# Performance work log

Measured on AMD Instinct MI355X. Metric: run time of the kernel, lower is better.

The kernel has to match this reference:

```python
import jax, jax.numpy as jnp
import numpy as np

EPS = 1e-5

def _ln(x, g, b):
    mu = jnp.mean(x, -1, keepdims=True)
    var = jnp.mean(jnp.square(x - mu), -1, keepdims=True)
    return (x - mu) * jax.lax.rsqrt(var + EPS) * g + b

def _switch_moe(h, gw, gb, W1, b1, W2, b2):
    # h: [B,T,D]; top-1 switch routing over E experts
    probs = jax.nn.softmax(h @ gw + gb, axis=-1)        # [B,T,E]
    idx = jnp.argmax(probs, axis=-1)                    # [B,T]
    p = jnp.max(probs, axis=-1)[..., None]              # [B,T,1] top-1 gate prob
    out = jnp.zeros_like(h)
    E = W1.shape[0]
    for e in range(E):  # small fixed expert count
        y = jax.nn.gelu(h @ W1[e] + b1[e]) @ W2[e] + b2[e]
        out = out + jnp.where((idx == e)[..., None], p * y, 0.0)
    return out

def setup_inputs() -> dict:
    key = jax.random.key(0)
    B, T, D, F, E, TE, NB = 64, 196, 512, 2048, 8, 512, 2
    ks = jax.random.split(key, 16)
    s = 0.02
    return {
        "x": jax.random.normal(ks[0], (B, T, D), jnp.float32),
        "emb": jax.random.normal(ks[1], (B, TE), jnp.float32),
        "ln_g": jnp.ones((NB, D), jnp.float32),
        "ln_b": jnp.zeros((NB, D), jnp.float32),
        "gate_w": jax.random.normal(ks[2], (NB, D, E), jnp.float32) * s,
        "gate_b": jnp.zeros((NB, E), jnp.float32),
        "w1": jax.random.normal(ks[3], (NB, E, D, F), jnp.float32) * s,
        "b1": jnp.zeros((NB, E, F), jnp.float32),
        "w2": jax.random.normal(ks[4], (NB, E, F, D), jnp.float32) * s,
        "b2": jnp.zeros((NB, E, D), jnp.float32),
        "emb_w": jax.random.normal(ks[5], (TE, 2 * D), jnp.float32) * s,
        "emb_b": jnp.zeros((2 * D,), jnp.float32),
        "sn_g": jnp.ones((D,), jnp.float32),
        "sn_b": jnp.zeros((D,), jnp.float32),
        "out_w": jax.random.normal(ks[6], (D, D), jnp.float32) * s,
        "out_b": jnp.zeros((D,), jnp.float32),
    }

def reference(x, emb, ln_g, ln_b, gate_w, gate_b, w1, b1, w2, b2,
              emb_w, emb_b, sn_g, sn_b, out_w, out_b):
    NB = ln_g.shape[0]
    out = jnp.zeros_like(x)
    for br in range(NB):  # fixed small branch count; dropout = identity (eval)
        h = _ln(x, ln_g[br], ln_b[br])
        out = out + _switch_moe(h, gate_w[br], gate_b[br], w1[br], b1[br], w2[br], b2[br])
    out = out / NB
    # StylizationBlock (FiLM): norm, scale/shift from time emb, SiLU+Linear, residual
    eo = jax.nn.silu(emb) @ emb_w + emb_b            # [B,2D]
    scale, shift = jnp.split(eo[:, None, :], 2, axis=-1)  # [B,1,D] each
    h = _ln(out, sn_g, sn_b) * (1.0 + scale) + shift
    h = jax.nn.silu(h) @ out_w + out_b
    return x + h
```

## Files before the change

kernel.cpp:

```cpp
#include <hip/hip_runtime.h>
#include <hip/hip_bf16.h>

typedef unsigned short u16;
typedef unsigned int u32;

typedef short bf16v8 __attribute__((ext_vector_type(8)));
typedef float f32v4 __attribute__((ext_vector_type(4)));

constexpr int BB   = 64;
constexpr int TT   = 196;
constexpr int NTOK = BB * TT;
constexpr int DD   = 512;
constexpr int FF   = 2048;
constexpr int EE   = 8;
constexpr int NBR  = 2;
constexpr int GE   = NBR * EE;
constexpr int MT128 = 212;
constexpr int NB_FRONT = 840 + NTOK / 4;

__device__ __forceinline__ u16 f2bf(float f) {
    union { float f; u32 u; } v; v.f = f;
    u32 r = v.u + 0x7fffu + ((v.u >> 16) & 1u);
    return (u16)(r >> 16);
}

__device__ __forceinline__ float bf2f(u32 u) {
    union { u32 u; float f; } v; v.u = u << 16; return v.f;
}

__device__ __forceinline__ float wave_sum(float v) {
    #pragma unroll
    for (int m = 32; m > 0; m >>= 1) v += __shfl_xor(v, m, 64);
    return v;
}

__device__ __forceinline__ float gelu_tanh(float v) {
    float y = 1.595769122f * v + 0.071354816f * (v * v * v);
    return v / (1.0f + __expf(-y));
}

__device__ __forceinline__ float silu(float v) {
    return v / (1.0f + __expf(-v));
}

__device__ __forceinline__ void gload16(const u16* g, u16* l) {
    typedef const __attribute__((address_space(1))) unsigned gv_t;
    typedef __attribute__((address_space(3))) unsigned lv_t;
    __builtin_amdgcn_global_load_lds((gv_t*)g, (lv_t*)l, 16, 0, 0);
}

__device__ __forceinline__ void bar() {
    asm volatile("" ::: "memory");
    __builtin_amdgcn_s_barrier();
    asm volatile("" ::: "memory");
}

#define ASM_VMCNT4 asm volatile("s_waitcnt vmcnt(4)" ::: "memory")
#define ASM_VMCNT0 asm volatile("s_waitcnt vmcnt(0)" ::: "memory")
#define ASM_LGKM0  asm volatile("s_waitcnt lgkmcnt(0)" ::: "memory")

__global__ __launch_bounds__(256) void front_kernel(
    const float* __restrict__ w1, u16* __restrict__ w1t,
    const float* __restrict__ w2, u16* __restrict__ w2t,
    const float* __restrict__ ow, u16* __restrict__ owt,
    const float* __restrict__ emb, const float* __restrict__ emb_w,
    const float* __restrict__ emb_b, float* __restrict__ eo,
    int* __restrict__ cnt,
    const float* __restrict__ x, const float* __restrict__ ln_g,
    const float* __restrict__ ln_b, const float* __restrict__ gate_w,
    const float* __restrict__ gate_b,
    u16* __restrict__ hA, u16* __restrict__ hB,
    int* __restrict__ idxb, float* __restrict__ pbuf)
{
    __shared__ __align__(16) float smem[2 * 64 * 69];
    int id = blockIdx.x;
    int t = threadIdx.x;

    if (id >= 840) {
        int wave = t >> 6, lane = t & 63;
        int tok = (id - 840) * 4 + wave;
        const float* xr = x + (size_t)tok * DD + lane * 8;
        float4 v0 = *(const float4*)xr;
        float4 v1 = *(const float4*)(xr + 4);
        float xs[8] = {v0.x, v0.y, v0.z, v0.w, v1.x, v1.y, v1.z, v1.w};
        float s = 0.f, ss = 0.f;
        #pragma unroll
        for (int i = 0; i < 8; ++i) { s += xs[i]; ss += xs[i] * xs[i]; }
        s = wave_sum(s); ss = wave_sum(ss);
        float mu = s * (1.0f / DD);
        float var = ss * (1.0f / DD) - mu * mu;
        float rstd = rsqrtf(var + 1e-5f);

        #pragma unroll
        for (int br = 0; br < NBR; ++br) {
            u16* hb = br ? hB : hA;
            float part[8] = {0, 0, 0, 0, 0, 0, 0, 0};
            u16 hu[8];
            #pragma unroll
            for (int i = 0; i < 8; ++i) {
                int d = lane * 8 + i;
                float g = ln_g[br * DD + d], b = ln_b[br * DD + d];
                float h = (xs[i] - mu) * rstd * g + b;
                hu[i] = f2bf(h);
                const float* gw = gate_w + ((size_t)br * DD + d) * EE;
                float4 g0 = *(const float4*)gw;
                float4 g1 = *(const float4*)(gw + 4);
                part[0] += h * g0.x; part[1] += h * g0.y; part[2] += h * g0.z; part[3] += h * g0.w;
                part[4] += h * g1.x; part[5] += h * g1.y; part[6] += h * g1.z; part[7] += h * g1.w;
            }
            uint4 pk;
            pk.x = (u32)hu[0] | ((u32)hu[1] << 16);
            pk.y = (u32)hu[2] | ((u32)hu[3] << 16);
            pk.z = (u32)hu[4] | ((u32)hu[5] << 16);
            pk.w = (u32)hu[6] | ((u32)hu[7] << 16);
            *(uint4*)(hb + (size_t)tok * DD + lane * 8) = pk;

            float logit[8];
            #pragma unroll
            for (int e = 0; e < 8; ++e)
                logit[e] = wave_sum(part[e]) + gate_b[br * EE + e];
            float m = logit[0]; int bi = 0;
            #pragma unroll
            for (int e = 1; e < 8; ++e)
                if (logit[e] > m) { m = logit[e]; bi = e; }
            float sum = 0.f;
            #pragma unroll
            for (int e = 0; e < 8; ++e) sum += __expf(logit[e] - m);
            if (lane == 0) {
                idxb[br * NTOK + tok] = bi;
                pbuf[br * NTOK + tok] = 1.0f / sum;
            }
        }
        return;
    }

    if (id >= 776) {
        float* se = smem;
        int id2 = id - 776;
        int cg = id2 & 3, bg = id2 >> 2;
        int b0 = bg * 4;
        int c0 = cg * 256 + t;
        for (int i = t; i < 4 * DD; i += 256) {
            int b = i >> 9, d = i & (DD - 1);
            se[b * DD + d] = silu(emb[(size_t)(b0 + b) * DD + d]);
        }
        __syncthreads();
        float acc[4] = {0, 0, 0, 0};
        for (int k = 0; k < DD; ++k) {
            float wv = emb_w[(size_t)k * 1024 + c0];
            #pragma unroll
            for (int b = 0; b < 4; ++b) acc[b] += se[b * DD + k] * wv;
        }
        float bb = emb_b[c0];
        #pragma unroll
        for (int b = 0; b < 4; ++b)
            eo[(size_t)(b0 + b) * 1024 + c0] = acc[b] + bb;
        return;
    }

    if (id == 0 && t < 16) cnt[t] = 0;

    const float* src; u16* dst; int C, Rfull, rowbase, c0, NIT;
    if (id < 512) {
        int e = id >> 5, cg = id & 31;
        src = w1 + (size_t)e * DD * FF; dst = w1t + (size_t)e * FF * DD;
        C = FF; Rfull = DD; rowbase = 0; c0 = cg * 64; NIT = 8;
    } else if (id < 768) {
        int sid = id - 512; int e = sid >> 4, rem = sid & 15;
        src = w2 + (size_t)e * FF * DD; dst = w2t + (size_t)e * FF * DD;
        C = DD; Rfull = FF; rowbase = (rem >> 3) * 1024; c0 = (rem & 7) * 64; NIT = 16;
    } else {
        int cg = id - 768;
        src = ow; dst = owt;
        C = DD; Rfull = DD; rowbase = 0; c0 = cg * 64; NIT = 8;
    }

    float (*tile)[64][69] = (float (*)[64][69])smem;
    int tx = t & 15, ty = t >> 4;
    int wc = t & 7, wr0 = t >> 3;

    {
        float4 v[4];
        #pragma unroll
        for (int j = 0; j < 4; ++j)
            v[j] = *(const float4*)&src[(size_t)(rowbase + ty + 16 * j) * C + c0 + tx * 4];
        #pragma unroll
        for (int j = 0; j < 4; ++j) {
            int row = ty + 16 * j;
            tile[0][row][tx * 4 + 0] = v[j].x;
            tile[0][row][tx * 4 + 1] = v[j].y;
            tile[0][row][tx * 4 + 2] = v[j].z;
            tile[0][row][tx * 4 + 3] = v[j].w;
        }
        __syncthreads();
    }

    for (int it = 0; it < NIT; ++it) {
        int cur = it & 1;
        bool pre = (it + 1 < NIT);
        float4 nv[4];
        if (pre) {
            #pragma unroll
            for (int j = 0; j < 4; ++j)
                nv[j] = *(const float4*)&src[(size_t)(rowbase + (it + 1) * 64 + ty + 16 * j) * C + c0 + tx * 4];
        }
        #pragma unroll
        for (int p = 0; p < 2; ++p) {
            int cc = wr0 + p * 32;
            u16 pk[8];
            #pragma unroll
            for (int i = 0; i < 8; ++i)
                pk[i] = f2bf(tile[cur][wc * 8 + i][cc]);
            uint4 vv;
            vv.x = (u32)pk[0] | ((u32)pk[1] << 16);
            vv.y = (u32)pk[2] | ((u32)pk[3] << 16);
            vv.z = (u32)pk[4] | ((u32)pk[5] << 16);
            vv.w = (u32)pk[6] | ((u32)pk[7] << 16);
            *(uint4*)&dst[(size_t)(c0 + cc) * Rfull + rowbase + it * 64 + wc * 8] = vv;
        }
        if (pre) {
            #pragma unroll
            for (int j = 0; j < 4; ++j) {
                int row = ty + 16 * j;
                tile[cur ^ 1][row][tx * 4 + 0] = nv[j].x;
                tile[cur ^ 1][row][tx * 4 + 1] = nv[j].y;
                tile[cur ^ 1][row][tx * 4 + 2] = nv[j].z;
                tile[cur ^ 1][row][tx * 4 + 3] = nv[j].w;
            }
        }
        __syncthreads();
    }
}

__global__ __launch_bounds__(256) void route_kernel(
    const int* __restrict__ idxb, int* __restrict__ cnt, int* __restrict__ list)
{
    __shared__ int lcnt[GE];
    __shared__ int gbase[GE];
    int tid = threadIdx.x;
    int t = blockIdx.x * 256 + tid;
    if (tid < GE) lcnt[tid] = 0;
    __syncthreads();
    int e0 = idxb[t];
    int e1 = EE + idxb[NTOK + t];
    int r0 = atomicAdd(&lcnt[e0], 1);
    int r1 = atomicAdd(&lcnt[e1], 1);
    __syncthreads();
    if (tid < GE) {
        int c = lcnt[tid];
        gbase[tid] = c ? atomicAdd(&cnt[tid], c) : 0;
    }
    __syncthreads();
    list[(size_t)e0 * NTOK + gbase[e0] + r0] = t;
    list[(size_t)e1 * NTOK + gbase[e1] + r1] = t;
}

__global__ void tilestart_kernel(const int* __restrict__ cnt, int* __restrict__ meta)
{
    int lane = threadIdx.x;
    if (lane < 16) {
        int pbv = 0;
        for (int k = 0; k < lane; ++k) pbv += cnt[k];
        meta[lane] = pbv;
    }
    if (lane == 16) {
        int n = 0;
        for (int k = 0; k < 16; ++k) n += (cnt[k] + 127) >> 7;
        meta[33] = n;
    }
    for (int j = lane; j < MT128; j += 64) {
        int ge = -1, start = 0, tt = 0;
        #pragma unroll
        for (int k = 0; k < 16; ++k) {
            int mt = (cnt[k] + 127) >> 7;
            if (ge < 0) {
                if (j < start + mt) { ge = k; tt = j - start; }
                else start += mt;
            }
        }
        if (ge >= 0) meta[64 + j] = (ge << 20) | tt;
    }
}

template<int MODE>
__global__ __launch_bounds__(256, 4) void gemm_tile(
    const u16* __restrict__ A0, const u16* __restrict__ A1,
    const u16* __restrict__ Bt,
    const int* __restrict__ meta, const int* __restrict__ cnt,
    const int* __restrict__ list, const float* __restrict__ pbuf,
    const float* __restrict__ bias,
    u16* __restrict__ uout, u16* __restrict__ moeout)
{
    constexpr int K = (MODE == 1) ? FF : DD;
    constexpr int N = (MODE == 0) ? FF : DD;
    constexpr int NSTEP = K / 32;

    __shared__ __align__(16) u16 As[2][128 * 32];
    __shared__ __align__(16) u16 Bs[2][128 * 32];
    __shared__ int rowtok[128];
    __shared__ float rowp[128];

    int ntile = blockIdx.x;
    int j = blockIdx.y;
    if (j >= meta[33]) return;
    int ev = meta[64 + j];
    int ge = ev >> 20;
    int rb = (ev & 0xfffff) << 7;
    int cnt_e = cnt[ge];
    int pb = meta[ge];

    int tid = threadIdx.x, wave = tid >> 6, lane = tid & 63;
    int wm = wave >> 1, wn = wave & 1;
    int fr = lane & 15, fq = lane >> 4;
    int r0 = wave * 16 + (lane >> 2);
    int sc = (lane & 3) ^ ((lane >> 3) & 3);

    const u16* Abase;
    if constexpr (MODE == 0) Abase = (ge >= 8) ? A1 : A0;
    else                     Abase = A0;
    const u16* Bte = Bt + (size_t)ge * FF * DD;

    const u16 *aSrc0, *aSrc1, *bSrc0, *bSrc1;
    if constexpr (MODE == 0) {
        int lb = ge * NTOK;
        int g0 = rb + r0, g1 = g0 + 64;
        int t0 = (g0 < cnt_e) ? list[lb + g0] : list[lb];
        int t1 = (g1 < cnt_e) ? list[lb + g1] : list[lb];
        aSrc0 = Abase + (size_t)t0 * K + sc * 8;
        aSrc1 = Abase + (size_t)t1 * K + sc * 8;
    } else {
        size_t base = (size_t)(pb + rb);
        aSrc0 = Abase + (base + r0) * (size_t)K + sc * 8;
        aSrc1 = Abase + (base + r0 + 64) * (size_t)K + sc * 8;
    }
    {
        int nrow = ntile * 128 + r0;
        bSrc0 = Bte + (size_t)nrow * K + sc * 8;
        bSrc1 = Bte + (size_t)(nrow + 64) * K + sc * 8;
    }

    if constexpr (MODE == 1) {
        if (tid < 128) {
            int g = rb + tid;
            int tk = (g < cnt_e) ? list[ge * NTOK + g] : -1;
            rowtok[tid] = tk;
            rowp[tid] = (tk >= 0) ? pbuf[(ge >> 3) * NTOK + tk] : 0.f;
        }
        ASM_LGKM0;
    }

    f32v4 acc[4][4];
    #pragma unroll
    for (int mi = 0; mi < 4; ++mi)
        #pragma unroll
        for (int ni = 0; ni < 4; ++ni)
            acc[mi][ni] = (f32v4){0.f, 0.f, 0.f, 0.f};

    int ch = fq ^ ((fr >> 1) & 3);

    gload16(aSrc0, &As[0][wave * 512]);
    gload16(aSrc1, &As[0][2048 + wave * 512]);
    gload16(bSrc0, &Bs[0][wave * 512]);
    gload16(bSrc1, &Bs[0][2048 + wave * 512]);
    aSrc0 += 32; aSrc1 += 32; bSrc0 += 32; bSrc1 += 32;

    #pragma unroll 2
    for (int t = 0; t < NSTEP; ++t) {
        const int cur = t & 1;
        if (t + 1 < NSTEP) {
            gload16(aSrc0, &As[cur ^ 1][wave * 512]);
            gload16(aSrc1, &As[cur ^ 1][2048 + wave * 512]);
            gload16(bSrc0, &Bs[cur ^ 1][wave * 512]);
            gload16(bSrc1, &Bs[cur ^ 1][2048 + wave * 512]);
            aSrc0 += 32; aSrc1 += 32; bSrc0 += 32; bSrc1 += 32;
            ASM_VMCNT4;
        } else {
            ASM_VMCNT0;
        }
        bar();

        bf16v8 af[4], bfr[4];
        #pragma unroll
        for (int mi = 0; mi < 4; ++mi)
            af[mi] = *(const bf16v8*)&As[cur][(wm * 64 + mi * 16 + fr) * 32 + ch * 8];
        #pragma unroll
        for (int ni = 0; ni < 4; ++ni)
            bfr[ni] = *(const bf16v8*)&Bs[cur][(wn * 64 + ni * 16 + fr) * 32 + ch * 8];
        #pragma unroll
        for (int mi = 0; mi < 4; ++mi)
            #pragma unroll
            for (int ni = 0; ni < 4; ++ni)
                acc[mi][ni] = __builtin_amdgcn_mfma_f32_16x16x32_bf16(
                    af[mi], bfr[ni], acc[mi][ni], 0, 0, 0);
        bar();
    }

    #pragma unroll
    for (int mi = 0; mi < 4; ++mi) {
        #pragma unroll
        for (int ni = 0; ni < 4; ++ni) {
            int col = ntile * 128 + wn * 64 + ni * 16 + fr;
            float bn = bias[(size_t)ge * N + col];
            #pragma unroll
            for (int r = 0; r < 4; ++r) {
                int rr = wm * 64 + mi * 16 + fq * 4 + r;
                float v = acc[mi][ni][r] + bn;
                if constexpr (MODE == 0) {
                    if (rb + rr < cnt_e)
                        uout[(size_t)(pb + rb + rr) * FF + col] = f2bf(gelu_tanh(v));
                } else {
                    int tok = rowtok[rr];
                    if (tok >= 0)
                        moeout[((size_t)(ge >> 3) * NTOK + tok) * DD + col] =
                            f2bf(v * rowp[rr]);
                }
            }
        }
    }
}

__global__ __launch_bounds__(256, 4) void gemm_out(
    const u16* __restrict__ A0, const u16* __restrict__ Bt,
    const float* __restrict__ bias,
    const float* __restrict__ xres, float* __restrict__ dout)
{
    constexpr int K = DD;
    constexpr int NSTEP = K / 32;

    __shared__ __align__(16) u16 As[2][128 * 32];
    __shared__ __align__(16) u16 Bs[2][128 * 32];

    int ntile = blockIdx.x;
    int rb = blockIdx.y * 128;

    int tid = threadIdx.x, wave = tid >> 6, lane = tid & 63;
    int wm = wave >> 1, wn = wave & 1;
    int fr = lane & 15, fq = lane >> 4;
    int r0 = wave * 16 + (lane >> 2);
    int sc = (lane & 3) ^ ((lane >> 3) & 3);

    const u16 *aSrc0, *aSrc1, *bSrc0, *bSrc1;
    aSrc0 = A0 + (size_t)(rb + r0) * K + sc * 8;
    aSrc1 = A0 + (size_t)(rb + r0 + 64) * K + sc * 8;
    {
        int nrow = ntile * 128 + r0;
        bSrc0 = Bt + (size_t)nrow * K + sc * 8;
        bSrc1 = Bt + (size_t)(nrow + 64) * K + sc * 8;
    }

    f32v4 acc[4][4];
    #pragma unroll
    for (int mi = 0; mi < 4; ++mi)
        #pragma unroll
        for (int ni = 0; ni < 4; ++ni)
            acc[mi][ni] = (f32v4){0.f, 0.f, 0.f, 0.f};

    int ch = fq ^ ((fr >> 1) & 3);

    gload16(aSrc0, &As[0][wave * 512]);
    gload16(aSrc1, &As[0][2048 + wave * 512]);
    gload16(bSrc0, &Bs[0][wave * 512]);
    gload16(bSrc1, &Bs[0][2048 + wave * 512]);
    aSrc0 += 32; aSrc1 += 32; bSrc0 += 32; bSrc1 += 32;

    #pragma unroll 2
    for (int t = 0; t < NSTEP; ++t) {
        const int cur = t & 1;
        if (t + 1 < NSTEP) {
            gload16(aSrc0, &As[cur ^ 1][wave * 512]);
            gload16(aSrc1, &As[cur ^ 1][2048 + wave * 512]);
            gload16(bSrc0, &Bs[cur ^ 1][wave * 512]);
            gload16(bSrc1, &Bs[cur ^ 1][2048 + wave * 512]);
            aSrc0 += 32; aSrc1 += 32; bSrc0 += 32; bSrc1 += 32;
            ASM_VMCNT4;
        } else {
            ASM_VMCNT0;
        }
        bar();

        bf16v8 af[4], bfr[4];
        #pragma unroll
        for (int mi = 0; mi < 4; ++mi)
            af[mi] = *(const bf16v8*)&As[cur][(wm * 64 + mi * 16 + fr) * 32 + ch * 8];
        #pragma unroll
        for (int ni = 0; ni < 4; ++ni)
            bfr[ni] = *(const bf16v8*)&Bs[cur][(wn * 64 + ni * 16 + fr) * 32 + ch * 8];
        #pragma unroll
        for (int mi = 0; mi < 4; ++mi)
            #pragma unroll
            for (int ni = 0; ni < 4; ++ni)
                acc[mi][ni] = __builtin_amdgcn_mfma_f32_16x16x32_bf16(
                    af[mi], bfr[ni], acc[mi][ni], 0, 0, 0);
        bar();
    }

    #pragma unroll
    for (int mi = 0; mi < 4; ++mi) {
        #pragma unroll
        for (int ni = 0; ni < 4; ++ni) {
            int col = ntile * 128 + wn * 64 + ni * 16 + fr;
            float bn = bias[col];
            #pragma unroll
            for (int r = 0; r < 4; ++r) {
                int rr = wm * 64 + mi * 16 + fq * 4 + r;
                size_t o = (size_t)(rb + rr) * DD + col;
                dout[o] = xres[o] + acc[mi][ni][r] + bn;
            }
        }
    }
}

__global__ __launch_bounds__(256) void stylize_kernel(
    const u16* __restrict__ moe, const float* __restrict__ eo,
    const float* __restrict__ sn_g, const float* __restrict__ sn_b,
    u16* __restrict__ sbuf)
{
    int wave = threadIdx.x >> 6, lane = threadIdx.x & 63;
    int tok = blockIdx.x * 4 + wave;
    int b = tok / TT;
    const u16* mr = moe + (size_t)tok * DD + lane * 8;
    const u16* mr2 = mr + (size_t)NTOK * DD;
    uint4 pa = *(const uint4*)mr;
    uint4 pb = *(const uint4*)mr2;
    float os[8];
    os[0] = (bf2f(pa.x & 0xffff) + bf2f(pb.x & 0xffff)) * 0.5f;
    os[1] = (bf2f(pa.x >> 16)    + bf2f(pb.x >> 16))    * 0.5f;
    os[2] = (bf2f(pa.y & 0xffff) + bf2f(pb.y & 0xffff)) * 0.5f;
    os[3] = (bf2f(pa.y >> 16)    + bf2f(pb.y >> 16))    * 0.5f;
    os[4] = (bf2f(pa.z & 0xffff) + bf2f(pb.z & 0xffff)) * 0.5f;
    os[5] = (bf2f(pa.z >> 16)    + bf2f(pb.z >> 16))    * 0.5f;
    os[6] = (bf2f(pa.w & 0xffff) + bf2f(pb.w & 0xffff)) * 0.5f;
    os[7] = (bf2f(pa.w >> 16)    + bf2f(pb.w >> 16))    * 0.5f;
    float s = 0.f, ss = 0.f;
    #pragma unroll
    for (int i = 0; i < 8; ++i) { s += os[i]; ss += os[i] * os[i]; }
    s = wave_sum(s); ss = wave_sum(ss);
    float mu = s * (1.0f / DD);
    float var = ss * (1.0f / DD) - mu * mu;
    float rstd = rsqrtf(var + 1e-5f);
    u16 hu[8];
    #pragma unroll
    for (int i = 0; i < 8; ++i) {
        int d = lane * 8 + i;
        float h = (os[i] - mu) * rstd * sn_g[d] + sn_b[d];
        float scv = eo[(size_t)b * 1024 + d];
        float shv = eo[(size_t)b * 1024 + DD + d];
        h = h * (1.0f + scv) + shv;
        hu[i] = f2bf(silu(h));
    }
    uint4 pk;
    pk.x = (u32)hu[0] | ((u32)hu[1] << 16);
    pk.y = (u32)hu[2] | ((u32)hu[3] << 16);
    pk.z = (u32)hu[4] | ((u32)hu[5] << 16);
    pk.w = (u32)hu[6] | ((u32)hu[7] << 16);
    *(uint4*)(sbuf + (size_t)tok * DD + lane * 8) = pk;
}

extern "C" void kernel_launch(void* const* d_in, const int* in_sizes, int n_in,
                              void* d_out, int out_size, void* d_ws, size_t ws_size,
                              hipStream_t stream)
{
    const float* x      = (const float*)d_in[0];
    const float* emb    = (const float*)d_in[1];
    const float* ln_g   = (const float*)d_in[2];
    const float* ln_b   = (const float*)d_in[3];
    const float* gate_w = (const float*)d_in[4];
    const float* gate_b = (const float*)d_in[5];
    const float* w1     = (const float*)d_in[6];
    const float* b1     = (const float*)d_in[7];
    const float* w2     = (const float*)d_in[8];
    const float* b2     = (const float*)d_in[9];
    const float* emb_w  = (const float*)d_in[10];
    const float* emb_b  = (const float*)d_in[11];
    const float* sn_g   = (const float*)d_in[12];
    const float* sn_b   = (const float*)d_in[13];
    const float* out_w  = (const float*)d_in[14];
    const float* out_b  = (const float*)d_in[15];
    (void)n_in; (void)in_sizes; (void)out_size; (void)ws_size;

    const size_t szW    = (size_t)GE * FF * DD * 2;
    const size_t szOwt  = (size_t)DD * DD * 2;
    const size_t szH    = (size_t)NTOK * DD * 2;
    const size_t szEo   = (size_t)BB * 2 * DD * 4;
    const size_t szP    = (size_t)NBR * NTOK * 4;
    const size_t szCnt  = 256, szMeta = 4096;
    const size_t szList = (size_t)GE * NTOK * 4;
    const size_t szU    = ((size_t)2 * NTOK + 256) * FF * 2;
    const size_t szM    = (size_t)2 * NTOK * DD * 2;

    auto align256 = [](size_t v) { return (v + 255) & ~(size_t)255; };
    char* w = (char*)d_ws;
    size_t off = 0;
    auto take = [&](size_t bytes) -> void* {
        void* p = w + off;
        off = align256(off + bytes);
        return p;
    };
    u16*   w1t  = (u16*)take(szW);
    u16*   w2t  = (u16*)take(szW);
    u16*   owt  = (u16*)take(szOwt);
    u16*   hA   = (u16*)take(szH);
    u16*   hB   = (u16*)take(szH);
    float* eo   = (float*)take(szEo);
    float* pbuf = (float*)take(szP);
    int*   idxb = (int*)take(szP);
    int*   cnt  = (int*)take(szCnt);
    int*   meta = (int*)take(szMeta);
    int*   list = (int*)take(szList);
    u16*   ubuf = (u16*)take(szU);
    u16*   moe  = (u16*)take(szM);

    front_kernel<<<NB_FRONT, 256, 0, stream>>>(w1, w1t, w2, w2t, out_w, owt,
                                               emb, emb_w, emb_b, eo, cnt,
                                               x, ln_g, ln_b, gate_w, gate_b,
                                               hA, hB, idxb, pbuf);

    route_kernel<<<NTOK / 256, 256, 0, stream>>>(idxb, cnt, list);
    tilestart_kernel<<<1, 64, 0, stream>>>(cnt, meta);

    gemm_tile<0><<<dim3(FF / 128, MT128), 256, 0, stream>>>(
        hA, hB, w1t, meta, cnt, list, nullptr, b1, ubuf, nullptr);
    gemm_tile<1><<<dim3(DD / 128, MT128), 256, 0, stream>>>(
        ubuf, nullptr, w2t, meta, cnt, list, pbuf, b2, nullptr, moe);

    stylize_kernel<<<NTOK / 4, 256, 0, stream>>>(moe, eo, sn_g, sn_b, hA);
    gemm_out<<<dim3(DD / 128, NTOK / 128), 256, 0, stream>>>(
        hA, owt, out_b, x, (float*)d_out);
}
```

Before: 332.4 us.

## Move w2/out_w transpose and time-embedding work into first expert GEMM launch

The front kernel now only transposes w1 and does the layernorm and gating. The w2 and out_w bf16 transposes and the time-embedding projection run as extra blocks appended to the grid of the first expert GEMM, so they overlap with it instead of lengthening the front stage. The w1 transpose block index is also remapped to spread experts across XCDs. The extra GEMM blocks share a char-based LDS buffer and use a simpler single-buffer transpose loop. The risk is contention with the GEMM blocks, and tail effects if those extra blocks are scheduled last.

```diff
diff --git a/kernel.cpp b/kernel.cpp
--- a/kernel.cpp
+++ b/kernel.cpp
@@ -16,7 +16,8 @@
 constexpr int NBR  = 2;
 constexpr int GE   = NBR * EE;
 constexpr int MT128 = 212;
-constexpr int NB_FRONT = 840 + NTOK / 4;
+constexpr int MTY0  = 233;
+constexpr int NB_FRONT = 512 + NTOK / 4;
 
 __device__ __forceinline__ u16 f2bf(float f) {
     union { float f; u32 u; } v; v.f = f;
@@ -59,12 +60,8 @@
 #define ASM_VMCNT0 asm volatile("s_waitcnt vmcnt(0)" ::: "memory")
 #define ASM_LGKM0  asm volatile("s_waitcnt lgkmcnt(0)" ::: "memory")
 
-__global__ __launch_bounds__(256) void front_kernel(
+__global__ __launch_bounds__(256) void front1_kernel(
     const float* __restrict__ w1, u16* __restrict__ w1t,
-    const float* __restrict__ w2, u16* __restrict__ w2t,
-    const float* __restrict__ ow, u16* __restrict__ owt,
-    const float* __restrict__ emb, const float* __restrict__ emb_w,
-    const float* __restrict__ emb_b, float* __restrict__ eo,
     int* __restrict__ cnt,
     const float* __restrict__ x, const float* __restrict__ ln_g,
     const float* __restrict__ ln_b, const float* __restrict__ gate_w,
@@ -72,13 +69,13 @@
     u16* __restrict__ hA, u16* __restrict__ hB,
     int* __restrict__ idxb, float* __restrict__ pbuf)
 {
-    __shared__ __align__(16) float smem[2 * 64 * 69];
+    __shared__ __align__(16) float tile[2][64][69];
     int id = blockIdx.x;
     int t = threadIdx.x;
 
-    if (id >= 840) {
+    if (id >= 512) {
         int wave = t >> 6, lane = t & 63;
-        int tok = (id - 840) * 4 + wave;
+        int tok = (id - 512) * 4 + wave;
         const float* xr = x + (size_t)tok * DD + lane * 8;
         float4 v0 = *(const float4*)xr;
         float4 v1 = *(const float4*)(xr + 4);
@@ -134,48 +131,16 @@
         return;
     }
 
-    if (id >= 776) {
-        float* se = smem;
-        int id2 = id - 776;
-        int cg = id2 & 3, bg = id2 >> 2;
-        int b0 = bg * 4;
-        int c0 = cg * 256 + t;
-        for (int i = t; i < 4 * DD; i += 256) {
-            int b = i >> 9, d = i & (DD - 1);
-            se[b * DD + d] = silu(emb[(size_t)(b0 + b) * DD + d]);
-        }
-        __syncthreads();
-        float acc[4] = {0, 0, 0, 0};
-        for (int k = 0; k < DD; ++k) {
-            float wv = emb_w[(size_t)k * 1024 + c0];
-            #pragma unroll
-            for (int b = 0; b < 4; ++b) acc[b] += se[b * DD + k] * wv;
-        }
-        float bb = emb_b[c0];
-        #pragma unroll
-        for (int b = 0; b < 4; ++b)
-            eo[(size_t)(b0 + b) * 1024 + c0] = acc[b] + bb;
-        return;
-    }
-
     if (id == 0 && t < 16) cnt[t] = 0;
 
-    const float* src; u16* dst; int C, Rfull, rowbase, c0, NIT;
-    if (id < 512) {
-        int e = id >> 5, cg = id & 31;
-        src = w1 + (size_t)e * DD * FF; dst = w1t + (size_t)e * FF * DD;
-        C = FF; Rfull = DD; rowbase = 0; c0 = cg * 64; NIT = 8;
-    } else if (id < 768) {
-        int sid = id - 512; int e = sid >> 4, rem = sid & 15;
-        src = w2 + (size_t)e * FF * DD; dst = w2t + (size_t)e * FF * DD;
-        C = DD; Rfull = FF; rowbase = (rem >> 3) * 1024; c0 = (rem & 7) * 64; NIT = 16;
-    } else {
-        int cg = id - 768;
-        src = ow; dst = owt;
-        C = DD; Rfull = DD; rowbase = 0; c0 = cg * 64; NIT = 8;
-    }
-
-    float (*tile)[64][69] = (float (*)[64][69])smem;
+    int xcd = id & 7;
+    int e = ((id >> 8) << 3) | xcd;
+    int cg = (id >> 3) & 31;
+    const float* src = w1 + (size_t)e * DD * FF;
+    u16* dst = w1t + (size_t)e * FF * DD;
+    const int C = FF, Rfull = DD, NIT = 8;
+    int c0 = cg * 64;
+
     int tx = t & 15, ty = t >> 4;
     int wc = t & 7, wr0 = t >> 3;
 
@@ -183,7 +148,7 @@
         float4 v[4];
         #pragma unroll
         for (int j = 0; j < 4; ++j)
-            v[j] = *(const float4*)&src[(size_t)(rowbase + ty + 16 * j) * C + c0 + tx * 4];
+            v[j] = *(const float4*)&src[(size_t)(ty + 16 * j) * C + c0 + tx * 4];
         #pragma unroll
         for (int j = 0; j < 4; ++j) {
             int row = ty + 16 * j;
@@ -202,7 +167,7 @@
         if (pre) {
             #pragma unroll
             for (int j = 0; j < 4; ++j)
-                nv[j] = *(const float4*)&src[(size_t)(rowbase + (it + 1) * 64 + ty + 16 * j) * C + c0 + tx * 4];
+                nv[j] = *(const float4*)&src[(size_t)((it + 1) * 64 + ty + 16 * j) * C + c0 + tx * 4];
         }
         #pragma unroll
         for (int p = 0; p < 2; ++p) {
@@ -216,7 +181,7 @@
             vv.y = (u32)pk[2] | ((u32)pk[3] << 16);
             vv.z = (u32)pk[4] | ((u32)pk[5] << 16);
             vv.w = (u32)pk[6] | ((u32)pk[7] << 16);
-            *(uint4*)&dst[(size_t)(c0 + cc) * Rfull + rowbase + it * 64 + wc * 8] = vv;
+            *(uint4*)&dst[(size_t)(c0 + cc) * Rfull + it * 64 + wc * 8] = vv;
         }
         if (pre) {
             #pragma unroll
@@ -289,27 +254,108 @@
     const int* __restrict__ meta, const int* __restrict__ cnt,
     const int* __restrict__ list, const float* __restrict__ pbuf,
     const float* __restrict__ bias,
-    u16* __restrict__ uout, u16* __restrict__ moeout)
+    u16* __restrict__ uout, u16* __restrict__ moeout,
+    const float* __restrict__ w2, u16* __restrict__ w2t,
+    const float* __restrict__ ow, u16* __restrict__ owt,
+    const float* __restrict__ emb, const float* __restrict__ emb_w,
+    const float* __restrict__ emb_b, float* __restrict__ eo)
 {
     constexpr int K = (MODE == 1) ? FF : DD;
     constexpr int N = (MODE == 0) ? FF : DD;
     constexpr int NSTEP = K / 32;
 
-    __shared__ __align__(16) u16 As[2][128 * 32];
-    __shared__ __align__(16) u16 Bs[2][128 * 32];
-    __shared__ int rowtok[128];
-    __shared__ float rowp[128];
-
+    __shared__ __align__(16) char smem[34304];
+    int tid = threadIdx.x;
     int ntile = blockIdx.x;
     int j = blockIdx.y;
+
+    if constexpr (MODE == 0) {
+        if (j >= MT128) {
+            int unit = (j - MT128) * 16 + ntile;
+            if (unit < 264) {
+                const float* src; u16* dst; int C, Rfull, rowbase, c0, NIT;
+                if (unit < 256) {
+                    int e = unit >> 4, rem = unit & 15;
+                    src = w2 + (size_t)e * FF * DD; dst = w2t + (size_t)e * FF * DD;
+                    C = DD; Rfull = FF; rowbase = (rem >> 3) * 1024; c0 = (rem & 7) * 64; NIT = 16;
+                } else {
+                    int cg = unit - 256;
+                    src = ow; dst = owt;
+                    C = DD; Rfull = DD; rowbase = 0; c0 = cg * 64; NIT = 8;
+                }
+                float (*tile)[69] = (float (*)[69])smem;
+                int tx = tid & 15, ty = tid >> 4;
+                int wc = tid & 7, wr0 = tid >> 3;
+                for (int it = 0; it < NIT; ++it) {
+                    float4 nv[4];
+                    #pragma unroll
+                    for (int jj = 0; jj < 4; ++jj)
+                        nv[jj] = *(const float4*)&src[(size_t)(rowbase + it * 64 + ty + 16 * jj) * C + c0 + tx * 4];
+                    __syncthreads();
+                    #pragma unroll
+                    for (int jj = 0; jj < 4; ++jj) {
+                        int row = ty + 16 * jj;
+                        tile[row][tx * 4 + 0] = nv[jj].x;
+                        tile[row][tx * 4 + 1] = nv[jj].y;
+                        tile[row][tx * 4 + 2] = nv[jj].z;
+                        tile[row][tx * 4 + 3] = nv[jj].w;
+                    }
+                    __syncthreads();
+                    #pragma unroll
+                    for (int p = 0; p < 2; ++p) {
+                        int cc = wr0 + p * 32;
+                        u16 pk[8];
+                        #pragma unroll
+                        for (int i = 0; i < 8; ++i)
+                            pk[i] = f2bf(tile[wc * 8 + i][cc]);
+                        uint4 vv;
+                        vv.x = (u32)pk[0] | ((u32)pk[1] << 16);
+                        vv.y = (u32)pk[2] | ((u32)pk[3] << 16);
+                        vv.z = (u32)pk[4] | ((u32)pk[5] << 16);
+                        vv.w = (u32)pk[6] | ((u32)pk[7] << 16);
+                        *(uint4*)&dst[(size_t)(c0 + cc) * Rfull + rowbase + it * 64 + wc * 8] = vv;
+                    }
+                }
+            } else if (unit < 328) {
+                float* se = (float*)smem;
+                int id2 = unit - 264;
+                int cg = id2 & 3, bg = id2 >> 2;
+                int b0 = bg * 4;
+                int c0 = cg * 256 + tid;
+                for (int i = tid; i < 4 * DD; i += 256) {
+                    int b = i >> 9, d = i & (DD - 1);
+                    se[b * DD + d] = silu(emb[(size_t)(b0 + b) * DD + d]);
+                }
+                __syncthreads();
+                float acc[4] = {0, 0, 0, 0};
+                for (int k = 0; k < DD; ++k) {
+                    float wv = emb_w[(size_t)k * 1024 + c0];
+                    #pragma unroll
+                    for (int b = 0; b < 4; ++b) acc[b] += se[b * DD + k] * wv;
+                }
+                float bb = emb_b[c0];
+                #pragma unroll
+                for (int b = 0; b < 4; ++b)
+                    eo[(size_t)(b0 + b) * 1024 + c0] = acc[b] + bb;
+            }
+            return;
+        }
+    }
+
     if (j >= meta[33]) return;
+
+    u16 (*As)[4096] = (u16 (*)[4096])smem;
+    u16 (*Bs)[4096] = (u16 (*)[4096])(smem + 16384);
+    int*   rowtok   = (int*)(smem + 32768);
+    float* rowp     = (float*)(smem + 33280);
+
     int ev = meta[64 + j];
     int ge = ev >> 20;
     int rb = (ev & 0xfffff) << 7;
     int cnt_e = cnt[ge];
     int pb = meta[ge];
 
-    int tid = threadIdx.x, wave = tid >> 6, lane = tid & 63;
+    int wave = tid >> 6, lane = tid & 63;
     int wm = wave >> 1, wn = wave & 1;
     int fr = lane & 15, fq = lane >> 4;
     int r0 = wave * 16 + (lane >> 2);
@@ -610,18 +656,19 @@
     u16*   ubuf = (u16*)take(szU);
     u16*   moe  = (u16*)take(szM);
 
-    front_kernel<<<NB_FRONT, 256, 0, stream>>>(w1, w1t, w2, w2t, out_w, owt,
-                                               emb, emb_w, emb_b, eo, cnt,
-                                               x, ln_g, ln_b, gate_w, gate_b,
-                                               hA, hB, idxb, pbuf);
+    front1_kernel<<<NB_FRONT, 256, 0, stream>>>(w1, w1t, cnt,
+                                                x, ln_g, ln_b, gate_w, gate_b,
+                                                hA, hB, idxb, pbuf);
 
     route_kernel<<<NTOK / 256, 256, 0, stream>>>(idxb, cnt, list);
     tilestart_kernel<<<1, 64, 0, stream>>>(cnt, meta);
 
-    gemm_tile<0><<<dim3(FF / 128, MT128), 256, 0, stream>>>(
-        hA, hB, w1t, meta, cnt, list, nullptr, b1, ubuf, nullptr);
+    gemm_tile<0><<<dim3(FF / 128, MTY0), 256, 0, stream>>>(
+        hA, hB, w1t, meta, cnt, list, nullptr, b1, ubuf, nullptr,
+        w2, w2t, out_w, owt, emb, emb_w, emb_b, eo);
     gemm_tile<1><<<dim3(DD / 128, MT128), 256, 0, stream>>>(
-        ubuf, nullptr, w2t, meta, cnt, list, pbuf, b2, nullptr, moe);
+        ubuf, nullptr, w2t, meta, cnt, list, pbuf, b2, nullptr, moe,
+        nullptr, nullptr, nullptr, nullptr, nullptr, nullptr, nullptr, nullptr);
 
     stylize_kernel<<<NTOK / 4, 256, 0, stream>>>(moe, eo, sn_g, sn_b, hA);
     gemm_out<<<dim3(DD / 128, NTOK / 128), 256, 0, stream>>>(
```

Measured after the change: 351.5 us. 5.7% more time.
